# Kernel optimization log

Measured on AMD Instinct MI355X. Metric: run time of the kernel, lower is better.

Reference implementation:

```python
import jax, jax.numpy as jnp
import numpy as np
from jax import lax

B, L, T = 16, 400, 200
N_MELS, ENC, PRE = 80, 512, 256
QH, DH, ATTN = 1024, 1024, 128
NFILT, K = 32, 31
PAD = (K - 1) // 2  # 15


def setup_inputs() -> dict:
    key = jax.random.key(0)
    ks = jax.random.split(key, 20)
    def w(k, shape, s=0.05):
        return jax.random.normal(k, shape, dtype=jnp.float32) * s
    return {
        "memory": w(ks[0], (B, L, ENC), 1.0),
        "memory_lengths": jnp.full((B,), L, dtype=jnp.int32),
        "teacher": w(ks[1], (B, T, N_MELS), 1.0),
        # prenet (Linear bias=False x2)
        "pre_w1": w(ks[2], (PRE, N_MELS)),
        "pre_w2": w(ks[3], (PRE, PRE)),
        # query_rnn LSTMCell (input = prenet_dim + enc_embed_dim)
        "q_wih": w(ks[4], (4 * QH, PRE + ENC)),
        "q_whh": w(ks[5], (4 * QH, QH)),
        "q_bih": jnp.zeros((4 * QH,), jnp.float32),
        "q_bhh": jnp.zeros((4 * QH,), jnp.float32),
        # dec_rnn LSTMCell (input = query_rnn_dim + enc_embed_dim)
        "d_wih": w(ks[6], (4 * DH, QH + ENC)),
        "d_whh": w(ks[7], (4 * DH, DH)),
        "d_bih": jnp.zeros((4 * DH,), jnp.float32),
        "d_bhh": jnp.zeros((4 * DH,), jnp.float32),
        # location-sensitive attention
        "attn_wq": w(ks[8], (ATTN, QH)),
        "attn_wm": w(ks[9], (ATTN, ENC)),
        "attn_conv": w(ks[10], (NFILT, 2, K)),  # Conv1d(2 -> NFILT, k=31), bias=False
        "attn_wloc": w(ks[11], (ATTN, NFILT)),
        "attn_v": w(ks[12], (1, ATTN)),
        # output projections
        "proj_w": w(ks[13], (N_MELS, DH + ENC)),
        "proj_b": jnp.zeros((N_MELS,), jnp.float32),
        "gate_w": w(ks[14], (1, DH + ENC)),
        "gate_b": jnp.zeros((1,), jnp.float32),
    }


def _prenet(x, w1, w2):
    # dropout p=0 -> identity
    x = jax.nn.relu(x @ w1.T)
    return jax.nn.relu(x @ w2.T)


def _lstm_cell(x, h, c, wih, whh, bih, bhh):
    z = x @ wih.T + h @ whh.T + bih + bhh
    i, f, g, o = jnp.split(z, 4, axis=-1)  # torch LSTMCell gate order
    c = jax.nn.sigmoid(f) * c + jax.nn.sigmoid(i) * jnp.tanh(g)
    h = jax.nn.sigmoid(o) * jnp.tanh(c)
    return h, c


def reference(memory, memory_lengths, teacher, pre_w1, pre_w2,
              q_wih, q_whh, q_bih, q_bhh, d_wih, d_whh, d_bih, d_bhh,
              attn_wq, attn_wm, attn_conv, attn_wloc, attn_v,
              proj_w, proj_b, gate_w, gate_b):
    del memory_lengths  # forward() sets mask = None unconditionally
    processed_memory = memory @ attn_wm.T            # (B, L, ATTN)

    # teacher-forced prenet inputs (tf_rate=1.0, drop_dec_in=0.0)
    go = _prenet(jnp.zeros((B, N_MELS), memory.dtype), pre_w1, pre_w2)  # (B, PRE)
    tpre = _prenet(teacher, pre_w1, pre_w2)          # (B, T, PRE)
    dec_ins = jnp.concatenate([go[:, None], tpre[:, :-1]], axis=1)       # (B, T, PRE)
    dec_ins = dec_ins.transpose(1, 0, 2)             # (T, B, PRE)

    z = lambda *s: jnp.zeros(s, memory.dtype)
    carry0 = (z(B, QH), z(B, QH), z(B, DH), z(B, DH), z(B, L), z(B, L), z(B, ENC))

    def step(carry, dec_in):
        qh, qc, dh, dc, aw, aws, ctx = carry
        qh, qc = _lstm_cell(jnp.concatenate([dec_in, ctx], -1), qh, qc,
                            q_wih, q_whh, q_bih, q_bhh)
        # location-sensitive attention
        hist = jnp.stack([aw, aws], axis=1)          # (B, 2, L)
        loc = lax.conv_general_dilated(hist, attn_conv, (1,), [(PAD, PAD)],
                                       dimension_numbers=("NCH", "OIH", "NCH"))  # (B, NFILT, L)
        loc = jnp.einsum("bfl,af->bla", loc, attn_wloc)          # (B, L, ATTN)
        pq = (qh @ attn_wq.T)[:, None, :]                         # (B, 1, ATTN)
        energies = jnp.tanh(pq + loc + processed_memory) @ attn_v[0]  # (B, L)
        weights = jax.nn.softmax(energies, axis=-1)               # (B, L)
        ctx = jnp.einsum("bl,ble->be", weights, memory)           # (B, ENC)
        aws = aws + weights
        dh, dc = _lstm_cell(jnp.concatenate([ctx, qh], -1), dh, dc,
                            d_wih, d_whh, d_bih, d_bhh)
        feat = jnp.concatenate([dh, ctx], -1)                     # (B, DH+ENC)
        mel = feat @ proj_w.T + proj_b                            # (B, N_MELS)
        stop = jax.nn.sigmoid(feat @ gate_w.T + gate_b)[:, 0]     # (B,)
        return (qh, qc, dh, dc, weights, aws, ctx), (mel, weights, stop)

    _, (mels, aligns, stops) = lax.scan(step, carry0, dec_ins)
    mel_outputs = mels.transpose(1, 0, 2)      # (B, T, n_mels)  (n_frames_per_step=1)
    alignments = aligns.transpose(1, 0, 2)     # (B, T, L)
    stops = stops.transpose(1, 0)              # (B, T)
    return mel_outputs, alignments, stops
```

## Files before the change

### kernel.cpp

```cpp
#include <hip/hip_runtime.h>
#include <math.h>

#define Bsz 16
#define Lsz 400
#define Tsz 200
#define NMELS 80
#define ENC 512
#define PREsz 256
#define QHsz 1024
#define DHsz 1024
#define ATTNsz 128
#define NFILT 32
#define KW 31
#define PADW 15

typedef const float* __restrict__ cfp;
typedef float* __restrict__ fp;
typedef __fp16 hf;
typedef __fp16 h2 __attribute__((ext_vector_type(2)));
typedef const hf* __restrict__ chp;

union F4H { float4 f; h2 h[4]; };

__device__ __forceinline__ float4 ldf4(const float* p){ return *reinterpret_cast<const float4*>(p); }
__device__ __forceinline__ float sigm(float x){ return 1.0f/(1.0f + __expf(-x)); }
__device__ __forceinline__ float tanhfast(float x){
  x = fminf(fmaxf(x, -15.0f), 15.0f);
  float e = __expf(2.0f*x);
  return (e-1.0f)/(e+1.0f);
}
__device__ __forceinline__ h2 pk2(float a, float b){
  return __builtin_amdgcn_cvt_pkrtz(a, b);
}
__device__ __forceinline__ float fdot2f(h2 a, h2 b, float c){
#if __has_builtin(__builtin_amdgcn_fdot2)
  return __builtin_amdgcn_fdot2(a, b, c, false);
#else
  return c + (float)a.x*(float)b.x + (float)a.y*(float)b.y;
#endif
}

__global__ void kzero(fp p, int n){
  int i = blockIdx.x*256 + threadIdx.x;
  if (i < n) p[i] = 0.0f;
}

__global__ void kcvt(cfp src, hf* __restrict__ dst, int n){
  int i = (blockIdx.x*256 + threadIdx.x)*4;
  if (i + 3 < n){
    float4 v = ldf4(src + i);
    dst[i+0] = (hf)v.x; dst[i+1] = (hf)v.y; dst[i+2] = (hf)v.z; dst[i+3] = (hf)v.w;
  } else {
    for (int k=i; k<n; k++) dst[k] = (hf)src[k];
  }
}

__global__ void kcvt_wq(cfp src, hf* __restrict__ dst){
  int idx = blockIdx.x*256 + threadIdx.x;
  int c = idx >> 8, rk = idx & 255;
  int r = rk >> 1, kh = rk & 1;
  const float* s = src + ((size_t)r*1024 + kh*512 + c*8);
  hf* d = dst + ((size_t)idx)*8;
  float4 v0 = ldf4(s), v1 = ldf4(s+4);
  d[0]=(hf)v0.x; d[1]=(hf)v0.y; d[2]=(hf)v0.z; d[3]=(hf)v0.w;
  d[4]=(hf)v1.x; d[5]=(hf)v1.y; d[6]=(hf)v1.z; d[7]=(hf)v1.w;
}

__global__ void __launch_bounds__(256) kprenet2(cfp teacher, cfp w1, cfp w2, fp dec_ins){
  int b = blockIdx.x & 15, tc = blockIdx.x >> 4;
  int t0 = tc*16;
  int tid = threadIdx.x;
  __shared__ __align__(16) float tch[16][80];
  __shared__ __align__(16) float h1[16][256];
  for (int idx = tid; idx < 16*80; idx += 256){
    int i = idx / 80, k = idx % 80;
    int t = t0 + i;
    float v = 0.f;
    if (t >= 1 && t < Tsz) v = teacher[((size_t)b*Tsz + (t-1))*NMELS + k];
    tch[i][k] = v;
  }
  __syncthreads();
  {
    int r = tid;
    float acc[16];
    #pragma unroll
    for (int i=0;i<16;i++) acc[i]=0.f;
    const float* wr = w1 + (size_t)r*80;
    for (int k=0;k<80;k++){
      float w = wr[k];
      #pragma unroll
      for (int i=0;i<16;i++) acc[i] += w * tch[i][k];
    }
    #pragma unroll
    for (int i=0;i<16;i++) h1[i][r] = fmaxf(acc[i], 0.f);
  }
  __syncthreads();
  {
    int r = tid;
    float acc[16];
    #pragma unroll
    for (int i=0;i<16;i++) acc[i]=0.f;
    const float* wr = w2 + (size_t)r*256;
    for (int k=0;k<256;k++){
      float w = wr[k];
      #pragma unroll
      for (int i=0;i<16;i++) acc[i] += w * h1[i][k];
    }
    for (int i=0;i<16;i++){
      int t = t0 + i;
      if (t < Tsz){
        float v = (t == 0) ? 0.f : fmaxf(acc[i], 0.f);
        dec_ins[((size_t)t*Bsz + b)*PREsz + r] = v;
      }
    }
  }
}

__global__ void __launch_bounds__(256) kpm2(cfp memory, cfp wm, fp pm){
  int b = blockIdx.x / 25, lc = blockIdx.x % 25;
  int l0 = lc*16;
  int tid = threadIdx.x;
  __shared__ __align__(16) float mrow[16][512];
  {
    const float4* s4 = (const float4*)(memory + ((size_t)b*Lsz + l0)*ENC);
    float4* d4 = (float4*)&mrow[0][0];
    #pragma unroll
    for (int i=0;i<8;i++) d4[tid + i*256] = s4[tid + i*256];
  }
  __syncthreads();
  int a = tid & 127, g = tid >> 7;
  const float* wr = wm + (size_t)a*ENC;
  float acc[8];
  #pragma unroll
  for (int i=0;i<8;i++) acc[i]=0.f;
  for (int k=0;k<512;k+=4){
    float4 w4 = ldf4(wr + k);
    #pragma unroll
    for (int i=0;i<8;i++){
      float4 x4 = ldf4(&mrow[g*8+i][k]);
      acc[i] += w4.x*x4.x + w4.y*x4.y + w4.z*x4.z + w4.w*x4.w;
    }
  }
  #pragma unroll
  for (int i=0;i<8;i++)
    pm[((size_t)b*Lsz + l0 + g*8 + i)*ATTNsz + a] = acc[i];
}

struct GateSmem { __align__(16) h2 xsh[16][132]; };
struct ConvSmem { float hists[2][80]; float convo[NFILT][50]; float cwsh[NFILT*2*KW]; float stat2[2]; };
union SMemA { GateSmem g; ConvSmem c; };

__global__ void __launch_bounds__(256) kgatesA(
    int t, int do_q, int do_d,
    cfp dec_ins, cfp qh_state, cfp dh_state,
    cfp cpartP, cfp emaxP, cfp esumP, cfp ebufP,
    cfp awsP, fp awsQ,
    fp qpart, fp dpart, fp loc, fp out_align,
    chp h_qwih, chp h_qwhh, chp h_dwih, chp h_dwhh,
    cfp conv_w, cfp wloc)
{
  int bid = blockIdx.x, tid = threadIdx.x;
  __shared__ SMemA sm;

  if (bid >= 144){
    int gid = bid - 144;
    int isq = (gid < 448);
    if (isq ? !do_q : !do_d) return;
    int idx = isq ? gid : (gid - 448);
    int nch = isq ? 7 : 10;
    int c = idx % nch, rg = idx / nch;
    int bb = tid >> 4, quar = tid & 15;
    int is_ctx = isq ? (c >= 1 && c <= 2) : (c <= 1);
    int ctxoff = isq ? (c-1)*256 : c*256;
    h2* dst = &sm.g.xsh[bb][quar*8];
    if (is_ctx){
      if (!do_d){
        h2 z = pk2(0.f, 0.f);
        #pragma unroll
        for (int i=0;i<8;i++) dst[i] = z;
      } else {
        float m0=emaxP[bb*4+0], m1=emaxP[bb*4+1], m2=emaxP[bb*4+2], m3=emaxP[bb*4+3];
        float gm = fmaxf(fmaxf(m0,m1), fmaxf(m2,m3));
        float e0=__expf(m0-gm), e1=__expf(m1-gm), e2=__expf(m2-gm), e3=__expf(m3-gm);
        float gs = esumP[bb*4+0]*e0 + esumP[bb*4+1]*e1 + esumP[bb*4+2]*e2 + esumP[bb*4+3]*e3;
        float inv = 1.0f/gs;
        float s0=e0*inv, s1=e1*inv, s2=e2*inv, s3=e3*inv;
        const float* cp = cpartP + (size_t)bb*2048 + ctxoff + quar*16;
        #pragma unroll
        for (int kk=0;kk<16;kk+=4){
          float4 p0 = ldf4(cp+kk), p1 = ldf4(cp+512+kk), p2 = ldf4(cp+1024+kk), p3 = ldf4(cp+1536+kk);
          float ax = s0*p0.x + s1*p1.x + s2*p2.x + s3*p3.x;
          float ay = s0*p0.y + s1*p1.y + s2*p2.y + s3*p3.y;
          float az = s0*p0.z + s1*p1.z + s2*p2.z + s3*p3.z;
          float aw = s0*p0.w + s1*p1.w + s2*p2.w + s3*p3.w;
          dst[(kk>>1)+0] = pk2(ax, ay);
          dst[(kk>>1)+1] = pk2(az, aw);
        }
      }
    } else {
      const float* src;
      if (isq){
        if (c == 0)      src = dec_ins + (size_t)t*Bsz*PREsz + bb*PREsz;
        else             src = qh_state + bb*QHsz + (c-3)*256;
      } else {
        if (c < 6)       src = qh_state + bb*QHsz + (c-2)*256;
        else             src = dh_state + bb*DHsz + (c-6)*256;
      }
      const float4* s4 = (const float4*)(src + quar*16);
      float4 t0=s4[0], t1=s4[1], t2=s4[2], t3=s4[3];
      dst[0]=pk2(t0.x,t0.y); dst[1]=pk2(t0.z,t0.w);
      dst[2]=pk2(t1.x,t1.y); dst[3]=pk2(t1.z,t1.w);
      dst[4]=pk2(t2.x,t2.y); dst[5]=pk2(t2.z,t2.w);
      dst[6]=pk2(t3.x,t3.y); dst[7]=pk2(t3.z,t3.w);
    }
    __syncthreads();
    int b = tid & 15, rl = tid >> 4;
    int row0 = rg*64 + rl*4;
    const hf* wbase; int wstride, woff;
    if (isq){
      if (c < 3){ wbase = h_qwih; wstride = 768;  woff = c*256; }
      else      { wbase = h_qwhh; wstride = 1024; woff = (c-3)*256; }
    } else {
      if (c < 6){ wbase = h_dwih; wstride = 1536; woff = c*256; }
      else      { wbase = h_dwhh; wstride = 1024; woff = (c-6)*256; }
    }
    const h2* w0 = (const h2*)(wbase + (size_t)(row0+0)*wstride + woff);
    const h2* w1 = (const h2*)(wbase + (size_t)(row0+1)*wstride + woff);
    const h2* w2 = (const h2*)(wbase + (size_t)(row0+2)*wstride + woff);
    const h2* w3 = (const h2*)(wbase + (size_t)(row0+3)*wstride + woff);
    const h2* xr = &sm.g.xsh[b][0];
    float a0=0.f, a1=0.f, a2=0.f, a3=0.f;
    #pragma unroll 1
    for (int kb=0; kb<128; kb+=8){
      F4H xA, xB;
      xA.f = ldf4((const float*)(xr + kb));
      xB.f = ldf4((const float*)(xr + kb + 4));
      F4H u0, u1, u2, u3;
      u0.f = ldf4((const float*)(w0 + kb));
      u1.f = ldf4((const float*)(w0 + kb + 4));
      u2.f = ldf4((const float*)(w1 + kb));
      u3.f = ldf4((const float*)(w1 + kb + 4));
      #pragma unroll
      for (int j=0;j<4;j++){
        a0 = fdot2f(u0.h[j], xA.h[j], a0);
        a0 = fdot2f(u1.h[j], xB.h[j], a0);
        a1 = fdot2f(u2.h[j], xA.h[j], a1);
        a1 = fdot2f(u3.h[j], xB.h[j], a1);
      }
      u0.f = ldf4((const float*)(w2 + kb));
      u1.f = ldf4((const float*)(w2 + kb + 4));
      u2.f = ldf4((const float*)(w3 + kb));
      u3.f = ldf4((const float*)(w3 + kb + 4));
      #pragma unroll
      for (int j=0;j<4;j++){
        a2 = fdot2f(u0.h[j], xA.h[j], a2);
        a2 = fdot2f(u1.h[j], xB.h[j], a2);
        a3 = fdot2f(u2.h[j], xA.h[j], a3);
        a3 = fdot2f(u3.h[j], xB.h[j], a3);
      }
    }
    float4 out = {a0, a1, a2, a3};
    fp part = isq ? qpart : dpart;
    *reinterpret_cast<float4*>(part + ((size_t)(c*16 + b))*4096 + row0) = out;
  } else if (bid < 128){
    if (!do_q) return;
    int cb = bid;
    int b = cb >> 3, chunk = cb & 7;
    int l0 = chunk*50;
    for (int i=tid; i<NFILT*2*KW; i+=256) sm.c.cwsh[i] = conv_w[i];
    if (tid == 0 && do_d){
      float m0=emaxP[b*4+0], m1=emaxP[b*4+1], m2=emaxP[b*4+2], m3=emaxP[b*4+3];
      float gm = fmaxf(fmaxf(m0,m1), fmaxf(m2,m3));
      float gs = esumP[b*4+0]*__expf(m0-gm) + esumP[b*4+1]*__expf(m1-gm)
               + esumP[b*4+2]*__expf(m2-gm) + esumP[b*4+3]*__expf(m3-gm);
      sm.c.stat2[0] = gm; sm.c.stat2[1] = 1.0f/gs;
    }
    __syncthreads();
    float gm = sm.c.stat2[0], ginv = sm.c.stat2[1];
    for (int i=tid; i<80; i+=256){
      int pos = l0 - PADW + i;
      float w = 0.f, as = 0.f;
      if (do_d && pos >= 0 && pos < Lsz){
        w = __expf(ebufP[b*Lsz + pos] - gm) * ginv;
        as = awsP[b*Lsz + pos] + w;
      }
      sm.c.hists[0][i] = w;
      sm.c.hists[1][i] = as;
    }
    __syncthreads();
    for (int task=tid; task<NFILT*50; task+=256){
      int f = task & 31, ll = task >> 5;
      float a = 0.0f;
      const float* c0 = &sm.c.cwsh[(f*2+0)*KW];
      const float* c1 = &sm.c.cwsh[(f*2+1)*KW];
      #pragma unroll
      for (int k=0;k<KW;k++) a += sm.c.hists[0][ll+k]*c0[k] + sm.c.hists[1][ll+k]*c1[k];
      sm.c.convo[f][ll] = a;
    }
    __syncthreads();
    for (int task=tid; task<50*ATTNsz; task+=256){
      int a = task & 127, ll = task >> 7;
      float s = 0.0f;
      const float* wl = wloc + a*NFILT;
      #pragma unroll
      for (int f=0;f<NFILT;f++) s += sm.c.convo[f][ll]*wl[f];
      loc[((size_t)b*Lsz + l0 + ll)*ATTNsz + a] = s;
    }
  } else {
    if (!do_d) return;
    int b = bid - 128;
    __shared__ float st2[2];
    if (tid == 0){
      float m0=emaxP[b*4+0], m1=emaxP[b*4+1], m2=emaxP[b*4+2], m3=emaxP[b*4+3];
      float gm = fmaxf(fmaxf(m0,m1), fmaxf(m2,m3));
      float gs = esumP[b*4+0]*__expf(m0-gm) + esumP[b*4+1]*__expf(m1-gm)
               + esumP[b*4+2]*__expf(m2-gm) + esumP[b*4+3]*__expf(m3-gm);
      st2[0] = gm; st2[1] = 1.0f/gs;
    }
    __syncthreads();
    float gm = st2[0], ginv = st2[1];
    for (int l=tid; l<Lsz; l+=256){
      float w = __expf(ebufP[b*Lsz + l] - gm) * ginv;
      awsQ[b*Lsz + l] = awsP[b*Lsz + l] + w;
      out_align[((size_t)b*Tsz + (t-1))*Lsz + l] = w;
    }
  }
}

__global__ void __launch_bounds__(256) kmidB(
    int t, int do_q, int do_d,
    cfp qpart, cfp dpart,
    cfp qcP, fp qcQ, fp qh_state,
    cfp dcP, fp dcQ, fp dh_state,
    chp h_wq, cfp vvec, cfp loc, cfp pm, cfp memory,
    cfp cpartP, cfp emaxP, cfp esumP,
    fp cpartQ, fp emaxQ, fp esumQ, fp ebufQ,
    cfp q_bih, cfp q_bhh, cfp d_bih, cfp d_bhh,
    chp h_proj, cfp proj_b, chp h_gate, cfp gate_b,
    fp out_mel, fp out_stop)
{
  int bid = blockIdx.x, tid = threadIdx.x;
  if (bid < 64){
    if (!do_q) return;
    int b = bid & 15, lc = bid >> 4;
    int l0 = lc*100;
    int lane = tid & 63, wv = tid >> 6;
    __shared__ __align__(16) h2 qh2l[512];
    __shared__ float pqv[128], vsh[128];
    __shared__ float esh[100], pesh[100];
    __shared__ float red4[4], red4b[4];
    __shared__ __align__(16) float4 psum[128];
    {
      int j4 = tid*4;
      float4 acc[4];
      #pragma unroll
      for (int g=0; g<4; g++){
        int r4 = g*1024 + j4;
        float4 bi = ldf4(q_bih + r4), bh = ldf4(q_bhh + r4);
        float4 a = {bi.x+bh.x, bi.y+bh.y, bi.z+bh.z, bi.w+bh.w};
        #pragma unroll
        for (int c=0;c<7;c++){
          float4 p = ldf4(qpart + ((size_t)(c*16 + b))*4096 + r4);
          a.x += p.x; a.y += p.y; a.z += p.z; a.w += p.w;
        }
        acc[g] = a;
      }
      float4 zi = acc[0], zf = acc[1], zg = acc[2], zo = acc[3];
      float4 cp = ldf4(qcP + b*QHsz + j4);
      float4 cn, hn;
      cn.x = sigm(zf.x)*cp.x + sigm(zi.x)*tanhfast(zg.x); hn.x = sigm(zo.x)*tanhfast(cn.x);
      cn.y = sigm(zf.y)*cp.y + sigm(zi.y)*tanhfast(zg.y); hn.y = sigm(zo.y)*tanhfast(cn.y);
      cn.z = sigm(zf.z)*cp.z + sigm(zi.z)*tanhfast(zg.z); hn.z = sigm(zo.z)*tanhfast(cn.z);
      cn.w = sigm(zf.w)*cp.w + sigm(zi.w)*tanhfast(zg.w); hn.w = sigm(zo.w)*tanhfast(cn.w);
      if (lc == 0){
        *reinterpret_cast<float4*>(qcQ + b*QHsz + j4) = cn;
        *reinterpret_cast<float4*>(qh_state + b*QHsz + j4) = hn;
      }
      qh2l[tid*2+0] = pk2(hn.x, hn.y);
      qh2l[tid*2+1] = pk2(hn.z, hn.w);
    }
    if (tid < 128) vsh[tid] = vvec[tid];
    __syncthreads();
    {
      int kh = tid & 1;
      const h2* wq2 = (const h2*)h_wq;
      const h2* xr = &qh2l[kh*256];
      int l4 = tid*4;
      float acc = 0.f;
      #pragma unroll 4
      for (int c=0;c<64;c+=2){
        F4H wA, wB, xA, xB;
        wA.f = ldf4((const float*)(wq2 + c*1024 + l4));
        wB.f = ldf4((const float*)(wq2 + (c+1)*1024 + l4));
        xA.f = ldf4((const float*)(xr + c*4));
        xB.f = ldf4((const float*)(xr + c*4 + 4));
        #pragma unroll
        for (int j=0;j<4;j++){
          acc = fdot2f(wA.h[j], xA.h[j], acc);
          acc = fdot2f(wB.h[j], xB.h[j], acc);
        }
      }
      acc += __shfl_xor(acc, 1, 64);
      if (kh == 0) pqv[tid >> 1] = acc;
    }
    __syncthreads();
    {
      int ll = tid >> 1, ah = tid & 1;
      float e = 0.f;
      if (ll < 100){
        int l = l0 + ll;
        const float* lp = loc + ((size_t)b*Lsz + l)*ATTNsz + ah*64;
        const float* pp = pm  + ((size_t)b*Lsz + l)*ATTNsz + ah*64;
        const float* pqa = &pqv[ah*64];
        const float* va  = &vsh[ah*64];
        #pragma unroll 4
        for (int a=0;a<64;a+=4){
          float4 l4 = ldf4(lp+a), p4 = ldf4(pp+a);
          e += tanhfast(pqa[a+0]+l4.x+p4.x)*va[a+0];
          e += tanhfast(pqa[a+1]+l4.y+p4.y)*va[a+1];
          e += tanhfast(pqa[a+2]+l4.z+p4.z)*va[a+2];
          e += tanhfast(pqa[a+3]+l4.w+p4.w)*va[a+3];
        }
      }
      e += __shfl_xor(e, 1, 64);
      if (ll < 100 && ah == 0) esh[ll] = e;
    }
    __syncthreads();
    {
      float lm = (tid < 100) ? esh[tid] : -1e30f;
      #pragma unroll
      for (int off=32; off>0; off>>=1) lm = fmaxf(lm, __shfl_xor(lm, off, 64));
      if (lane == 0) red4[wv] = lm;
      __syncthreads();
      float mx = fmaxf(fmaxf(red4[0], red4[1]), fmaxf(red4[2], red4[3]));
      float p = 0.f;
      if (tid < 100){
        p = __expf(esh[tid]-mx);
        pesh[tid] = p;
        ebufQ[b*Lsz + l0 + tid] = esh[tid];
      }
      float ls = p;
      #pragma unroll
      for (int off=32; off>0; off>>=1) ls += __shfl_xor(ls, off, 64);
      if (lane == 0) red4b[wv] = ls;
      __syncthreads();
      if (tid == 0){
        emaxQ[b*4+lc] = mx;
        esumQ[b*4+lc] = red4b[0]+red4b[1]+red4b[2]+red4b[3];
      }
    }
    {
      int e4 = tid & 127, lh = tid >> 7;
      const float* mp = memory + ((size_t)b*Lsz + l0)*ENC + e4*4;
      float4 a = {0.f,0.f,0.f,0.f};
      for (int l = lh*50; l < lh*50+50; l++){
        float w = pesh[l];
        float4 m4 = ldf4(mp + (size_t)l*ENC);
        a.x += w*m4.x; a.y += w*m4.y; a.z += w*m4.z; a.w += w*m4.w;
      }
      if (lh == 1) psum[e4] = a;
      __syncthreads();
      if (lh == 0){
        float4 p = psum[e4];
        a.x += p.x; a.y += p.y; a.z += p.z; a.w += p.w;
        *reinterpret_cast<float4*>(cpartQ + ((size_t)b*4 + lc)*512 + e4*4) = a;
      }
    }
  } else {
    if (!do_d) return;
    int db = bid - 64;
    int b = db & 15, half = db >> 4;
    int tm = t - 1;
    int lane = tid & 63, wv = tid >> 6;
    __shared__ __align__(16) h2 feath[768];
    __shared__ float scs[4];
    {
      int j4 = tid*4;
      float4 acc[4];
      #pragma unroll
      for (int g=0; g<4; g++){
        int r4 = g*1024 + j4;
        float4 bi = ldf4(d_bih + r4), bh = ldf4(d_bhh + r4);
        float4 a = {bi.x+bh.x, bi.y+bh.y, bi.z+bh.z, bi.w+bh.w};
        #pragma unroll
        for (int c=0;c<10;c++){
          float4 p = ldf4(dpart + ((size_t)(c*16 + b))*4096 + r4);
          a.x += p.x; a.y += p.y; a.z += p.z; a.w += p.w;
        }
        acc[g] = a;
      }
      if (tid == 0){
        float m0=emaxP[b*4+0], m1=emaxP[b*4+1], m2=emaxP[b*4+2], m3=emaxP[b*4+3];
        float gm = fmaxf(fmaxf(m0,m1), fmaxf(m2,m3));
        float e0=__expf(m0-gm), e1=__expf(m1-gm), e2=__expf(m2-gm), e3=__expf(m3-gm);
        float gs = esumP[b*4+0]*e0 + esumP[b*4+1]*e1 + esumP[b*4+2]*e2 + esumP[b*4+3]*e3;
        float inv = 1.0f/gs;
        scs[0]=e0*inv; scs[1]=e1*inv; scs[2]=e2*inv; scs[3]=e3*inv;
      }
      float4 zi = acc[0], zf = acc[1], zg = acc[2], zo = acc[3];
      float4 cp = ldf4(dcP + b*DHsz + j4);
      float4 cn, hn;
      cn.x = sigm(zf.x)*cp.x + sigm(zi.x)*tanhfast(zg.x); hn.x = sigm(zo.x)*tanhfast(cn.x);
      cn.y = sigm(zf.y)*cp.y + sigm(zi.y)*tanhfast(zg.y); hn.y = sigm(zo.y)*tanhfast(cn.y);
      cn.z = sigm(zf.z)*cp.z + sigm(zi.z)*tanhfast(zg.z); hn.z = sigm(zo.z)*tanhfast(cn.z);
      cn.w = sigm(zf.w)*cp.w + sigm(zi.w)*tanhfast(zg.w); hn.w = sigm(zo.w)*tanhfast(cn.w);
      if (half == 0){
        *reinterpret_cast<float4*>(dcQ + b*DHsz + j4) = cn;
        *reinterpret_cast<float4*>(dh_state + b*DHsz + j4) = hn;
      }
      feath[tid*2+0] = pk2(hn.x, hn.y);
      feath[tid*2+1] = pk2(hn.z, hn.w);
    }
    __syncthreads();
    {
      float s0=scs[0], s1=scs[1], s2=scs[2], s3=scs[3];
      int i0 = tid*2;
      const float* cp = cpartP + (size_t)b*2048;
      float v0 = s0*cp[i0]   + s1*cp[512+i0]   + s2*cp[1024+i0]   + s3*cp[1536+i0];
      float v1 = s0*cp[i0+1] + s1*cp[512+i0+1] + s2*cp[1024+i0+1] + s3*cp[1536+i0+1];
      feath[512 + tid] = pk2(v0, v1);
    }
    __syncthreads();
    int rbeg = half*40, rend = half ? 81 : 40;
    for (int r = rbeg + wv; r < rend; r += 4){
      const h2* wr = (r < 80) ? (const h2*)(h_proj + (size_t)r*1536) : (const h2*)h_gate;
      float acc = 0.0f;
      #pragma unroll
      for (int m=0;m<3;m++){
        int k4 = (lane + 64*m)*4;
        F4H w, x;
        w.f = ldf4((const float*)(wr + k4));
        x.f = ldf4((const float*)(&feath[k4]));
        #pragma unroll
        for (int j=0;j<4;j++) acc = fdot2f(w.h[j], x.h[j], acc);
      }
      #pragma unroll
      for (int off=32; off>0; off>>=1) acc += __shfl_xor(acc, off, 64);
      if (lane == 0){
        if (r < 80) out_mel[((size_t)b*Tsz + tm)*NMELS + r] = acc + proj_b[r];
        else        out_stop[b*Tsz + tm] = sigm(acc + gate_b[0]);
      }
    }
  }
}

extern "C" void kernel_launch(void* const* d_in, const int* in_sizes, int n_in,
                              void* d_out, int out_size, void* d_ws, size_t ws_size,
                              hipStream_t stream)
{
  const float* memory  = (const float*)d_in[0];
  const float* teacher = (const float*)d_in[2];
  const float* pre_w1  = (const float*)d_in[3];
  const float* pre_w2  = (const float*)d_in[4];
  const float* q_wih   = (const float*)d_in[5];
  const float* q_whh   = (const float*)d_in[6];
  const float* q_bih   = (const float*)d_in[7];
  const float* q_bhh   = (const float*)d_in[8];
  const float* d_wih   = (const float*)d_in[9];
  const float* d_whh   = (const float*)d_in[10];
  const float* d_bih   = (const float*)d_in[11];
  const float* d_bhh   = (const float*)d_in[12];
  const float* attn_wq   = (const float*)d_in[13];
  const float* attn_wm   = (const float*)d_in[14];
  const float* attn_conv = (const float*)d_in[15];
  const float* attn_wloc = (const float*)d_in[16];
  const float* attn_v    = (const float*)d_in[17];
  const float* proj_w  = (const float*)d_in[18];
  const float* proj_b  = (const float*)d_in[19];
  const float* gate_w  = (const float*)d_in[20];
  const float* gate_b  = (const float*)d_in[21];

  float* ws = (float*)d_ws;
  float* dec_ins  = ws;
  float* pm       = dec_ins + 819200;
  float* loc      = pm + 819200;
  float* qpart    = loc + 819200;
  float* dpart    = qpart + 458752;
  float* ebuf2    = dpart + 655360;
  float* emax2    = ebuf2 + 12800;
  float* esum2    = emax2 + 128;
  float* cpart2   = esum2 + 128;
  float* qh_state = cpart2 + 65536;
  float* dh_state = qh_state + 16384;
  float* qc2      = dh_state + 16384;
  float* dc2      = qc2 + 32768;
  float* aws2     = dc2 + 32768;
  float* fend     = aws2 + 12800;

  hf* h_qwih = (hf*)fend;
  hf* h_qwhh = h_qwih + 3145728;
  hf* h_dwih = h_qwhh + 4194304;
  hf* h_dwhh = h_dwih + 6291456;
  hf* h_wq   = h_dwhh + 4194304;
  hf* h_proj = h_wq + 131072;
  hf* h_gate = h_proj + 122880;

  float* out_mel   = (float*)d_out;
  float* out_align = out_mel + (size_t)Bsz*Tsz*NMELS;
  float* out_stop  = out_align + (size_t)Bsz*Tsz*Lsz;

  const int stateN = 16384+16384+32768+32768+12800;
  kzero<<<dim3((stateN+255)/256), dim3(256), 0, stream>>>(qh_state, stateN);
  kcvt<<<dim3(3145728/1024), dim3(256), 0, stream>>>(q_wih, h_qwih, 3145728);
  kcvt<<<dim3(4194304/1024), dim3(256), 0, stream>>>(q_whh, h_qwhh, 4194304);
  kcvt<<<dim3(6291456/1024), dim3(256), 0, stream>>>(d_wih, h_dwih, 6291456);
  kcvt<<<dim3(4194304/1024), dim3(256), 0, stream>>>(d_whh, h_dwhh, 4194304);
  kcvt_wq<<<dim3(64), dim3(256), 0, stream>>>(attn_wq, h_wq);
  kcvt<<<dim3(122880/1024), dim3(256), 0, stream>>>(proj_w, h_proj, 122880);
  kcvt<<<dim3(2), dim3(256), 0, stream>>>(gate_w, h_gate, 1536);
  kprenet2<<<dim3(16*13), dim3(256), 0, stream>>>(teacher, pre_w1, pre_w2, dec_ins);
  kpm2<<<dim3(400), dim3(256), 0, stream>>>(memory, attn_wm, pm);

  for (int t = 0; t <= Tsz; t++){
    int pp = (t+1)&1, qq = t&1;
    int do_q = (t < Tsz) ? 1 : 0;
    int do_d = (t > 0) ? 1 : 0;
    kgatesA<<<dim3(1232), dim3(256), 0, stream>>>(
      t, do_q, do_d,
      dec_ins, qh_state, dh_state,
      cpart2 + pp*32768, emax2 + pp*64, esum2 + pp*64, ebuf2 + pp*6400,
      aws2 + pp*6400, aws2 + qq*6400,
      qpart, dpart, loc, out_align,
      h_qwih, h_qwhh, h_dwih, h_dwhh,
      attn_conv, attn_wloc);
    kmidB<<<dim3(96), dim3(256), 0, stream>>>(
      t, do_q, do_d,
      qpart, dpart,
      qc2 + pp*16384, qc2 + qq*16384, qh_state,
      dc2 + pp*16384, dc2 + qq*16384, dh_state,
      h_wq, attn_v, loc, pm, memory,
      cpart2 + pp*32768, emax2 + pp*64, esum2 + pp*64,
      cpart2 + qq*32768, emax2 + qq*64, esum2 + qq*64, ebuf2 + qq*6400,
      q_bih, q_bhh, d_bih, d_bhh,
      h_proj, proj_b, h_gate, gate_b,
      out_mel, out_stop);
  }
}
```

Before: 8.839 ms.

## Widen gate GEMV rows per thread, fold pm into loc, use fp16 memory

The gate GEMV blocks now compute 8 rows per thread instead of 4, which halves the block count in kgatesA (1232 to 688) and reuses each shared-memory x load across more weights. The processed-memory term is added into loc inside the conv stage, so the energy kernel reads one array instead of two. The encoder memory is also converted once to fp16 and the context reduction reads that copy, halving its bytes. The trade-offs are fewer resident blocks and less latency hiding in the GEMV, plus fp16 rounding in the context sum.

```diff
diff --git a/kernel.cpp b/kernel.cpp
--- a/kernel.cpp
+++ b/kernel.cpp
@@ -21,6 +21,7 @@
 typedef const hf* __restrict__ chp;
 
 union F4H { float4 f; h2 h[4]; };
+union F2H4 { float2 f; hf h[4]; };
 
 __device__ __forceinline__ float4 ldf4(const float* p){ return *reinterpret_cast<const float4*>(p); }
 __device__ __forceinline__ float sigm(float x){ return 1.0f/(1.0f + __expf(-x)); }
@@ -157,16 +158,16 @@
     cfp awsP, fp awsQ,
     fp qpart, fp dpart, fp loc, fp out_align,
     chp h_qwih, chp h_qwhh, chp h_dwih, chp h_dwhh,
-    cfp conv_w, cfp wloc)
+    cfp conv_w, cfp wloc, cfp pm)
 {
   int bid = blockIdx.x, tid = threadIdx.x;
   __shared__ SMemA sm;
 
   if (bid >= 144){
     int gid = bid - 144;
-    int isq = (gid < 448);
+    int isq = (gid < 224);
     if (isq ? !do_q : !do_d) return;
-    int idx = isq ? gid : (gid - 448);
+    int idx = isq ? gid : (gid - 224);
     int nch = isq ? 7 : 10;
     int c = idx % nch, rg = idx / nch;
     int bb = tid >> 4, quar = tid & 15;
@@ -215,7 +216,7 @@
     }
     __syncthreads();
     int b = tid & 15, rl = tid >> 4;
-    int row0 = rg*64 + rl*4;
+    int row0 = rg*128 + rl*8;
     const hf* wbase; int wstride, woff;
     if (isq){
       if (c < 3){ wbase = h_qwih; wstride = 768;  woff = c*256; }
@@ -224,44 +225,38 @@
       if (c < 6){ wbase = h_dwih; wstride = 1536; woff = c*256; }
       else      { wbase = h_dwhh; wstride = 1024; woff = (c-6)*256; }
     }
-    const h2* w0 = (const h2*)(wbase + (size_t)(row0+0)*wstride + woff);
-    const h2* w1 = (const h2*)(wbase + (size_t)(row0+1)*wstride + woff);
-    const h2* w2 = (const h2*)(wbase + (size_t)(row0+2)*wstride + woff);
-    const h2* w3 = (const h2*)(wbase + (size_t)(row0+3)*wstride + woff);
     const h2* xr = &sm.g.xsh[b][0];
-    float a0=0.f, a1=0.f, a2=0.f, a3=0.f;
+    float acc[8];
+    #pragma unroll
+    for (int r=0;r<8;r++) acc[r]=0.f;
     #pragma unroll 1
     for (int kb=0; kb<128; kb+=8){
       F4H xA, xB;
       xA.f = ldf4((const float*)(xr + kb));
       xB.f = ldf4((const float*)(xr + kb + 4));
-      F4H u0, u1, u2, u3;
-      u0.f = ldf4((const float*)(w0 + kb));
-      u1.f = ldf4((const float*)(w0 + kb + 4));
-      u2.f = ldf4((const float*)(w1 + kb));
-      u3.f = ldf4((const float*)(w1 + kb + 4));
-      #pragma unroll
-      for (int j=0;j<4;j++){
-        a0 = fdot2f(u0.h[j], xA.h[j], a0);
-        a0 = fdot2f(u1.h[j], xB.h[j], a0);
-        a1 = fdot2f(u2.h[j], xA.h[j], a1);
-        a1 = fdot2f(u3.h[j], xB.h[j], a1);
-      }
-      u0.f = ldf4((const float*)(w2 + kb));
-      u1.f = ldf4((const float*)(w2 + kb + 4));
-      u2.f = ldf4((const float*)(w3 + kb));
-      u3.f = ldf4((const float*)(w3 + kb + 4));
-      #pragma unroll
-      for (int j=0;j<4;j++){
-        a2 = fdot2f(u0.h[j], xA.h[j], a2);
-        a2 = fdot2f(u1.h[j], xB.h[j], a2);
-        a3 = fdot2f(u2.h[j], xA.h[j], a3);
-        a3 = fdot2f(u3.h[j], xB.h[j], a3);
-      }
-    }
-    float4 out = {a0, a1, a2, a3};
+      #pragma unroll
+      for (int r=0;r<8;r+=2){
+        const h2* wa = (const h2*)(wbase + (size_t)(row0+r)*wstride + woff);
+        const h2* wb = (const h2*)(wbase + (size_t)(row0+r+1)*wstride + woff);
+        F4H u0, u1, u2, u3;
+        u0.f = ldf4((const float*)(wa + kb));
+        u1.f = ldf4((const float*)(wa + kb + 4));
+        u2.f = ldf4((const float*)(wb + kb));
+        u3.f = ldf4((const float*)(wb + kb + 4));
+        #pragma unroll
+        for (int j=0;j<4;j++){
+          acc[r]   = fdot2f(u0.h[j], xA.h[j], acc[r]);
+          acc[r]   = fdot2f(u1.h[j], xB.h[j], acc[r]);
+          acc[r+1] = fdot2f(u2.h[j], xA.h[j], acc[r+1]);
+          acc[r+1] = fdot2f(u3.h[j], xB.h[j], acc[r+1]);
+        }
+      }
+    }
     fp part = isq ? qpart : dpart;
-    *reinterpret_cast<float4*>(part + ((size_t)(c*16 + b))*4096 + row0) = out;
+    float4 o0 = {acc[0], acc[1], acc[2], acc[3]};
+    float4 o1 = {acc[4], acc[5], acc[6], acc[7]};
+    *reinterpret_cast<float4*>(part + ((size_t)(c*16 + b))*4096 + row0) = o0;
+    *reinterpret_cast<float4*>(part + ((size_t)(c*16 + b))*4096 + row0 + 4) = o1;
   } else if (bid < 128){
     if (!do_q) return;
     int cb = bid;
@@ -304,7 +299,8 @@
       const float* wl = wloc + a*NFILT;
       #pragma unroll
       for (int f=0;f<NFILT;f++) s += sm.c.convo[f][ll]*wl[f];
-      loc[((size_t)b*Lsz + l0 + ll)*ATTNsz + a] = s;
+      size_t gi = ((size_t)b*Lsz + l0 + ll)*ATTNsz + a;
+      loc[gi] = s + pm[gi];
     }
   } else {
     if (!do_d) return;
@@ -332,7 +328,7 @@
     cfp qpart, cfp dpart,
     cfp qcP, fp qcQ, fp qh_state,
     cfp dcP, fp dcQ, fp dh_state,
-    chp h_wq, cfp vvec, cfp loc, cfp pm, cfp memory,
+    chp h_wq, cfp vvec, cfp loc, chp h_mem, cfp memory,
     cfp cpartP, cfp emaxP, cfp esumP,
     fp cpartQ, fp emaxQ, fp esumQ, fp ebufQ,
     cfp q_bih, cfp q_bhh, cfp d_bih, cfp d_bhh,
@@ -410,16 +406,15 @@
       if (ll < 100){
         int l = l0 + ll;
         const float* lp = loc + ((size_t)b*Lsz + l)*ATTNsz + ah*64;
-        const float* pp = pm  + ((size_t)b*Lsz + l)*ATTNsz + ah*64;
         const float* pqa = &pqv[ah*64];
         const float* va  = &vsh[ah*64];
         #pragma unroll 4
         for (int a=0;a<64;a+=4){
-          float4 l4 = ldf4(lp+a), p4 = ldf4(pp+a);
-          e += tanhfast(pqa[a+0]+l4.x+p4.x)*va[a+0];
-          e += tanhfast(pqa[a+1]+l4.y+p4.y)*va[a+1];
-          e += tanhfast(pqa[a+2]+l4.z+p4.z)*va[a+2];
-          e += tanhfast(pqa[a+3]+l4.w+p4.w)*va[a+3];
+          float4 l4 = ldf4(lp+a);
+          e += tanhfast(pqa[a+0]+l4.x)*va[a+0];
+          e += tanhfast(pqa[a+1]+l4.y)*va[a+1];
+          e += tanhfast(pqa[a+2]+l4.z)*va[a+2];
+          e += tanhfast(pqa[a+3]+l4.w)*va[a+3];
         }
       }
       e += __shfl_xor(e, 1, 64);
@@ -451,12 +446,13 @@
     }
     {
       int e4 = tid & 127, lh = tid >> 7;
-      const float* mp = memory + ((size_t)b*Lsz + l0)*ENC + e4*4;
+      const hf* mp = h_mem + ((size_t)b*Lsz + l0)*ENC + e4*4;
       float4 a = {0.f,0.f,0.f,0.f};
       for (int l = lh*50; l < lh*50+50; l++){
         float w = pesh[l];
-        float4 m4 = ldf4(mp + (size_t)l*ENC);
-        a.x += w*m4.x; a.y += w*m4.y; a.z += w*m4.z; a.w += w*m4.w;
+        F2H4 m; m.f = *reinterpret_cast<const float2*>(mp + (size_t)l*ENC);
+        a.x += w*(float)m.h[0]; a.y += w*(float)m.h[1];
+        a.z += w*(float)m.h[2]; a.w += w*(float)m.h[3];
       }
       if (lh == 1) psum[e4] = a;
       __syncthreads();
@@ -594,6 +590,7 @@
   hf* h_wq   = h_dwhh + 4194304;
   hf* h_proj = h_wq + 131072;
   hf* h_gate = h_proj + 122880;
+  hf* h_mem  = h_gate + 1536;
 
   float* out_mel   = (float*)d_out;
   float* out_align = out_mel + (size_t)Bsz*Tsz*NMELS;
@@ -608,6 +605,7 @@
   kcvt_wq<<<dim3(64), dim3(256), 0, stream>>>(attn_wq, h_wq);
   kcvt<<<dim3(122880/1024), dim3(256), 0, stream>>>(proj_w, h_proj, 122880);
   kcvt<<<dim3(2), dim3(256), 0, stream>>>(gate_w, h_gate, 1536);
+  kcvt<<<dim3(3276800/1024), dim3(256), 0, stream>>>(memory, h_mem, 3276800);
   kprenet2<<<dim3(16*13), dim3(256), 0, stream>>>(teacher, pre_w1, pre_w2, dec_ins);
   kpm2<<<dim3(400), dim3(256), 0, stream>>>(memory, attn_wm, pm);
 
@@ -615,20 +613,20 @@
     int pp = (t+1)&1, qq = t&1;
     int do_q = (t < Tsz) ? 1 : 0;
     int do_d = (t > 0) ? 1 : 0;
-    kgatesA<<<dim3(1232), dim3(256), 0, stream>>>(
+    kgatesA<<<dim3(688), dim3(256), 0, stream>>>(
       t, do_q, do_d,
       dec_ins, qh_state, dh_state,
       cpart2 + pp*32768, emax2 + pp*64, esum2 + pp*64, ebuf2 + pp*6400,
       aws2 + pp*6400, aws2 + qq*6400,
       qpart, dpart, loc, out_align,
       h_qwih, h_qwhh, h_dwih, h_dwhh,
-      attn_conv, attn_wloc);
+      attn_conv, attn_wloc, pm);
     kmidB<<<dim3(96), dim3(256), 0, stream>>>(
       t, do_q, do_d,
       qpart, dpart,
       qc2 + pp*16384, qc2 + qq*16384, qh_state,
       dc2 + pp*16384, dc2 + qq*16384, dh_state,
-      h_wq, attn_v, loc, pm, memory,
+      h_wq, attn_v, loc, h_mem, memory,
       cpart2 + pp*32768, emax2 + pp*64, esum2 + pp*64,
       cpart2 + qq*32768, emax2 + qq*64, esum2 + qq*64, ebuf2 + qq*6400,
       q_bih, q_bhh, d_bih, d_bhh,
```

After: 8.665 ms. 1.02x faster.
